# Kernel optimization log

Measured on AMD Instinct MI355X. Metric: run time of the kernel, lower is better.

The kernel has to match this reference:

```python
import jax, jax.numpy as jnp
import numpy as np

G = 32          # num graphs
NPG = 512       # nodes per graph
EPG = 4096      # edges per graph
DN = 128        # node/edge feat dim
DP = 64         # node identifier dim d_p
DE_ID = 64      # type identifier dim d_e
H = 768         # hidden_dim
IN_DIM = DN + 2 * DP + DE_ID  # 320


def setup_inputs() -> dict:
    key = jax.random.key(0)
    ks = jax.random.split(key, 9)
    N = G * NPG
    E = G * EPG
    x = jax.random.normal(ks[0], (N, DN), jnp.float32)
    edge_attr = jax.random.normal(ks[1], (E, DN), jnp.float32)
    P = jax.random.normal(ks[2], (N, DP), jnp.float32)  # ORF node identifiers
    E_V = jax.random.normal(ks[3], (1, DE_ID), jnp.float32) * 0.1
    E_E = jax.random.normal(ks[4], (1, DE_ID), jnp.float32) * 0.1
    W = jax.random.normal(ks[5], (H, IN_DIM), jnp.float32) / np.sqrt(IN_DIM)
    b = jnp.zeros((H,), jnp.float32)
    graph_token = jax.random.normal(ks[6], (1, H), jnp.float32) * 0.1
    # edges stay within their graph and are sorted by graph id
    base = jnp.repeat(jnp.arange(G, dtype=jnp.int32) * NPG, EPG)  # [E]
    src = base + jax.random.randint(ks[7], (E,), 0, NPG, jnp.int32)
    dst = base + jax.random.randint(ks[8], (E,), 0, NPG, jnp.int32)
    edge_index = jnp.stack([src, dst], axis=0)  # [2, E]
    batch = jnp.repeat(jnp.arange(G, dtype=jnp.int32), NPG)  # [N]
    return {
        "x": x, "edge_attr": edge_attr, "P": P,
        "E_V": E_V, "E_E": E_E, "W": W, "b": b, "graph_token": graph_token,
        "edge_index": edge_index, "batch": batch,
        "num_graphs": G, "max_node_num": NPG, "max_edge_num": EPG,
    }


def reference(x, edge_attr, P, E_V, E_E, W, b, graph_token,
              edge_index, batch, num_graphs, max_node_num, max_edge_num):
    N = x.shape[0]
    E = edge_index.shape[1]
    Hd = W.shape[0]
    d_e = E_V.shape[1]

    # node tokens: [x | P | P | E_V] @ W^T + b
    X_v = jnp.concatenate([x, P, P, jnp.broadcast_to(E_V, (N, d_e))], axis=1)
    X_v_proj = X_v @ W.T + b  # [N, H]

    # edge tokens: [edge_attr | P_u | P_v | E_E] @ W^T + b
    P_u = P[edge_index[0]]
    P_v = P[edge_index[1]]
    X_e = jnp.concatenate([edge_attr, P_u, P_v, jnp.broadcast_to(E_E, (E, d_e))], axis=1)
    X_e_proj = X_e @ W.T + b  # [E, H]

    # ragged -> padded packing (replaces per-graph python loop)
    ones_n = jnp.ones((N,), jnp.int32)
    node_num = jax.ops.segment_sum(ones_n, batch, num_segments=num_graphs)  # [G]
    node_ptr = jnp.cumsum(node_num) - node_num  # exclusive prefix sum
    node_pos = jnp.arange(N, dtype=jnp.int32) - node_ptr[batch]  # position within graph

    edge_batch = batch[edge_index[0]]  # [E]
    ones_e = jnp.ones((E,), jnp.int32)
    edge_num = jax.ops.segment_sum(ones_e, edge_batch, num_segments=num_graphs)
    edge_ptr = jnp.cumsum(edge_num) - edge_num
    edge_pos = jnp.arange(E, dtype=jnp.int32) - edge_ptr[edge_batch]

    seq_len = 1 + max_node_num + max_edge_num  # +1 for [graph] token
    tokens = jnp.zeros((num_graphs, seq_len, Hd), X_v_proj.dtype)
    tokens = tokens.at[:, 0, :].set(graph_token[0])
    tokens = tokens.at[batch, 1 + node_pos].set(X_v_proj)
    tokens = tokens.at[edge_batch, 1 + max_node_num + edge_pos].set(X_e_proj)

    attention_masks = jnp.zeros((num_graphs, seq_len), bool)
    attention_masks = attention_masks.at[:, 0].set(True)
    attention_masks = attention_masks.at[batch, 1 + node_pos].set(True)
    attention_masks = attention_masks.at[edge_batch, 1 + max_node_num + edge_pos].set(True)

    return tokens, attention_masks
```

## Files before the change

kernel.cpp:

```cpp
#include <hip/hip_runtime.h>
#include <stdint.h>

#define NG   32
#define NPG  512
#define EPG  4096
#define DN   128
#define DP   64
#define NN   (NG*NPG)
#define NE   (NG*EPG)
#define KD   320
#define HD   768
#define SEQ  (1+NPG+EPG)
#define TOK_ELEMS ((size_t)NG*SEQ*HD)
#define MASK_ELEMS ((size_t)NG*SEQ)

typedef unsigned short u16;
typedef __attribute__((ext_vector_type(8))) __bf16 bf16x8;
typedef __attribute__((ext_vector_type(8))) short  s16x8;
typedef __attribute__((ext_vector_type(4))) float  f32x4;

__device__ __forceinline__ u16 f2bf(float f) {
    uint32_t u = __builtin_bit_cast(uint32_t, f);
    u += 0x7fffu + ((u >> 16) & 1u);
    return (u16)(u >> 16);
}

__device__ __forceinline__ int b_off(int row, int kb) {
    return ((row >> 1) << 7) + ((row & 1) << 6) + (kb ^ (((row >> 1) & 3) << 4));
}

__global__ void ptr_k(const int* __restrict__ batch, const int* __restrict__ eidx,
                      int* __restrict__ nptr, int* __restrict__ eptr) {
    int t = threadIdx.x;
    if (t < NG) {
        int g = t, lo = 0, hi = NN;
        while (lo < hi) { int mid = (lo + hi) >> 1; if (batch[mid] < g) lo = mid + 1; else hi = mid; }
        nptr[g] = lo;
    } else if (t < 2 * NG) {
        int g = t - NG, lo = 0, hi = NE;
        while (lo < hi) { int mid = (lo + hi) >> 1; if (batch[eidx[mid]] < g) lo = mid + 1; else hi = mid; }
        eptr[g] = lo;
    }
}

__global__ void wconv_k(const float* __restrict__ W, u16* __restrict__ Wb) {
    int i = blockIdx.x * 256 + threadIdx.x;
    if (i < KD * HD) Wb[i] = f2bf(W[i]);
}

__global__ void aux_k(const float* __restrict__ gt, float* __restrict__ out) {
    size_t i = (size_t)blockIdx.x * 256 + threadIdx.x;
    if (i < (size_t)NG * HD) {
        int g = (int)(i / HD), c = (int)(i % HD);
        out[(size_t)g * SEQ * HD + c] = gt[c];
    } else {
        size_t m = i - (size_t)NG * HD;
        if (m < MASK_ELEMS) out[TOK_ELEMS + m] = 1.0f;
    }
}

__global__ __launch_bounds__(256, 2)
void gemm_scatter(const float* __restrict__ x,  const float* __restrict__ ea,
                  const float* __restrict__ P,  const float* __restrict__ EV,
                  const float* __restrict__ EEv,const float* __restrict__ bias,
                  const int* __restrict__ eidx, const int* __restrict__ batch,
                  const u16* __restrict__ Wb,   const int* __restrict__ nptr,
                  const int* __restrict__ eptr, float* __restrict__ out)
{
    __shared__ __align__(16) char b_lds[2][16384];
    __shared__ int info_src[128], info_pu[128], info_pv[128], info_orow[128];

    const int tid  = threadIdx.x;
    const int lane = tid & 63;
    const int wid  = tid >> 6;
    const int lrow = lane & 15;
    const int lq   = lane >> 4;

    uint32_t g_off[4], l_off[4];
    #pragma unroll
    for (int i = 0; i < 4; ++i) {
        uint32_t u = (uint32_t)(i * 256 + tid);
        g_off[i] = (u >> 3) * (KD * 2) + (u & 7) * 16;
        l_off[i] = (((u >> 2) & 1) * 8192u) + (uint32_t)b_off(u >> 3, (u & 3) * 16);
    }
    const char* WbB = (const char*)Wb;

    const int r0  = blockIdx.x * 128;
    const bool isNode = (r0 < NN);
    const float* feat = isNode ? x  : ea;
    const float* idv  = isNode ? EV : EEv;

    if (tid < 128) {
        int r = r0 + tid;
        if (isNode) {
            int g = batch[r];
            info_src[tid] = r; info_pu[tid] = r; info_pv[tid] = r;
            info_orow[tid] = g * SEQ + 1 + (r - nptr[g]);
        } else {
            int e = r - NN;
            int s = eidx[e], d = eidx[NE + e];
            int g = batch[s];
            info_src[tid] = e; info_pu[tid] = s; info_pv[tid] = d;
            info_orow[tid] = g * SEQ + 1 + NPG + (e - eptr[g]);
        }
    }
    __syncthreads();

    bf16x8 afr[2][10];
    int obase[2][4];
    #pragma unroll
    for (int rb = 0; rb < 2; ++rb) {
        const int arow = wid * 32 + rb * 16 + lrow;
        const int fsrc = info_src[arow];
        const int pu   = info_pu[arow];
        const int pv   = info_pv[arow];
        #pragma unroll
        for (int s = 0; s < 10; ++s) {
            const int kg = s * 32 + lq * 8;
            const float* sp;
            if      (s < 4) sp = feat + (size_t)fsrc * DN + kg;
            else if (s < 6) sp = P + (size_t)pu * DP + (kg - DN);
            else if (s < 8) sp = P + (size_t)pv * DP + (kg - DN - DP);
            else            sp = idv + (kg - DN - 2 * DP);
            f32x4 f0 = *reinterpret_cast<const f32x4*>(sp);
            f32x4 f1 = *reinterpret_cast<const f32x4*>(sp + 4);
            s16x8 v;
            v[0]=(short)f2bf(f0[0]); v[1]=(short)f2bf(f0[1]);
            v[2]=(short)f2bf(f0[2]); v[3]=(short)f2bf(f0[3]);
            v[4]=(short)f2bf(f1[0]); v[5]=(short)f2bf(f1[1]);
            v[6]=(short)f2bf(f1[2]); v[7]=(short)f2bf(f1[3]);
            afr[rb][s] = __builtin_bit_cast(bf16x8, v);
        }
        #pragma unroll
        for (int j = 0; j < 4; ++j)
            obase[rb][j] = info_orow[wid * 32 + rb * 16 + lq * 4 + j] * HD;
    }

    const int roff = b_off(lrow, lq * 16);

    s16x8 pre[4];
    #pragma unroll
    for (int i = 0; i < 4; ++i)
        pre[i] = *reinterpret_cast<const s16x8*>(WbB + g_off[i]);

    int cur = 0;
    int nxt = 1;
    for (int nt = 0; nt < 6; ++nt) {
        const int n0 = nt * 128;
        f32x4 acc[2][8];
        #pragma unroll
        for (int rb = 0; rb < 2; ++rb)
            #pragma unroll
            for (int i = 0; i < 8; ++i) acc[rb][i] = (f32x4)0.f;

        #pragma unroll
        for (int kp = 0; kp < 5; ++kp) {
            cur ^= 1;
            char* bb = &b_lds[0][0] + cur * 16384;
            #pragma unroll
            for (int i = 0; i < 4; ++i)
                *reinterpret_cast<s16x8*>(bb + l_off[i]) = pre[i];
            {
                int tn  = (nxt < 30) ? nxt : 29; ++nxt;
                int ntn = tn / 5, kpn = tn - ntn * 5;
                const char* gb = WbB + (size_t)ntn * (128 * KD * 2) + kpn * 128;
                #pragma unroll
                for (int i = 0; i < 4; ++i)
                    pre[i] = *reinterpret_cast<const s16x8*>(gb + g_off[i]);
            }
            asm volatile("s_waitcnt lgkmcnt(0)" ::: "memory");
            __builtin_amdgcn_sched_barrier(0);
            __builtin_amdgcn_s_barrier();
            #pragma unroll
            for (int kk = 0; kk < 2; ++kk) {
                const int kt = kp * 2 + kk;
                const char* bs = bb + kk * 8192;
                #pragma unroll
                for (int ni = 0; ni < 8; ++ni) {
                    bf16x8 bf = *reinterpret_cast<const bf16x8*>(bs + ni * 1024 + roff);
                    acc[0][ni] = __builtin_amdgcn_mfma_f32_16x16x32_bf16(afr[0][kt], bf, acc[0][ni], 0, 0, 0);
                    acc[1][ni] = __builtin_amdgcn_mfma_f32_16x16x32_bf16(afr[1][kt], bf, acc[1][ni], 0, 0, 0);
                }
            }
        }

        #pragma unroll
        for (int ni = 0; ni < 8; ++ni) {
            float bv = bias[n0 + ni * 16 + lrow];
            #pragma unroll
            for (int rb = 0; rb < 2; ++rb)
                #pragma unroll
                for (int j = 0; j < 4; ++j)
                    out[obase[rb][j] + n0 + ni * 16 + lrow] = acc[rb][ni][j] + bv;
        }
    }
}

extern "C" void kernel_launch(void* const* d_in, const int* in_sizes, int n_in,
                              void* d_out, int out_size, void* d_ws, size_t ws_size,
                              hipStream_t stream) {
    const float* x    = (const float*)d_in[0];
    const float* ea   = (const float*)d_in[1];
    const float* P    = (const float*)d_in[2];
    const float* EV   = (const float*)d_in[3];
    const float* EEv  = (const float*)d_in[4];
    const float* W    = (const float*)d_in[5];
    const float* bias = (const float*)d_in[6];
    const float* gt   = (const float*)d_in[7];
    const int* eidx   = (const int*)d_in[8];
    const int* batch  = (const int*)d_in[9];

    float* out = (float*)d_out;
    u16* Wb  = (u16*)d_ws;
    int* ints = (int*)((char*)d_ws + (size_t)KD * HD * 2);
    int *nptr = ints, *eptr = ints + 32;

    ptr_k<<<1, 64, 0, stream>>>(batch, eidx, nptr, eptr);
    wconv_k<<<(KD * HD + 255) / 256, 256, 0, stream>>>(W, Wb);
    aux_k<<<(int)(((size_t)NG * HD + MASK_ELEMS + 255) / 256), 256, 0, stream>>>(gt, out);
    gemm_scatter<<<dim3((NN + NE) / 128), 256, 0, stream>>>(
        x, ea, P, EV, EEv, bias, eidx, batch, Wb, nptr, eptr, out);
}
```

Baseline: 169.3 us.

## Halve N-tile to 64 and interleave previous tile's stores with next tile's MFMAs

The GEMM N-tile shrinks from 128 to 64 columns, so the LDS B buffer is halved and the prefetch schedule now walks 60 stages instead of 30. Two accumulator sets ping-pong, and the epilogue stores of the previous 64-column tile are spread across the five k-steps of the current tile, so global writes overlap MFMA work instead of forming a separate store burst. This is meant to hide the large output-write cost, at the price of more barriers per block and less B reuse per LDS load.

After: 169.0 us. Within noise of the previous version (-0.2%).

```diff
diff --git a/kernel.cpp b/kernel.cpp
--- a/kernel.cpp
+++ b/kernel.cpp
@@ -67,7 +67,7 @@
                   const u16* __restrict__ Wb,   const int* __restrict__ nptr,
                   const int* __restrict__ eptr, float* __restrict__ out)
 {
-    __shared__ __align__(16) char b_lds[2][16384];
+    __shared__ __align__(16) char b_lds[2][8192];
     __shared__ int info_src[128], info_pu[128], info_pv[128], info_orow[128];
 
     const int tid  = threadIdx.x;
@@ -76,12 +76,13 @@
     const int lrow = lane & 15;
     const int lq   = lane >> 4;
 
-    uint32_t g_off[4], l_off[4];
-    #pragma unroll
-    for (int i = 0; i < 4; ++i) {
+    uint32_t g_off[2], l_off[2];
+    #pragma unroll
+    for (int i = 0; i < 2; ++i) {
         uint32_t u = (uint32_t)(i * 256 + tid);
-        g_off[i] = (u >> 3) * (KD * 2) + (u & 7) * 16;
-        l_off[i] = (((u >> 2) & 1) * 8192u) + (uint32_t)b_off(u >> 3, (u & 3) * 16);
+        uint32_t row = u >> 3, c = u & 7;
+        g_off[i] = row * (KD * 2) + c * 16;
+        l_off[i] = ((c >> 2) * 4096u) + (uint32_t)b_off((int)row, (int)((c & 3) * 16));
     }
     const char* WbB = (const char*)Wb;
 
@@ -138,34 +139,41 @@
 
     const int roff = b_off(lrow, lq * 16);
 
-    s16x8 pre[4];
-    #pragma unroll
-    for (int i = 0; i < 4; ++i)
+    s16x8 pre[2];
+    #pragma unroll
+    for (int i = 0; i < 2; ++i)
         pre[i] = *reinterpret_cast<const s16x8*>(WbB + g_off[i]);
 
     int cur = 0;
     int nxt = 1;
-    for (int nt = 0; nt < 6; ++nt) {
-        const int n0 = nt * 128;
-        f32x4 acc[2][8];
+
+    constexpr int S0[5] = {0, 7, 14, 20, 26};
+    constexpr int S1[5] = {7, 14, 20, 26, 32};
+
+    auto do_nt = [&](f32x4 (&acc)[2][4], float (&bv)[4],
+                     f32x4 (&accP)[2][4], float (&bvP)[4],
+                     int n0, int pn0) {
         #pragma unroll
         for (int rb = 0; rb < 2; ++rb)
             #pragma unroll
-            for (int i = 0; i < 8; ++i) acc[rb][i] = (f32x4)0.f;
+            for (int i = 0; i < 4; ++i) acc[rb][i] = (f32x4)0.f;
+        #pragma unroll
+        for (int ni = 0; ni < 4; ++ni)
+            bv[ni] = bias[n0 + ni * 16 + lrow];
 
         #pragma unroll
         for (int kp = 0; kp < 5; ++kp) {
             cur ^= 1;
-            char* bb = &b_lds[0][0] + cur * 16384;
+            char* bb = &b_lds[0][0] + cur * 8192;
             #pragma unroll
-            for (int i = 0; i < 4; ++i)
+            for (int i = 0; i < 2; ++i)
                 *reinterpret_cast<s16x8*>(bb + l_off[i]) = pre[i];
             {
-                int tn  = (nxt < 30) ? nxt : 29; ++nxt;
+                int tn  = (nxt < 60) ? nxt : 59; ++nxt;
                 int ntn = tn / 5, kpn = tn - ntn * 5;
-                const char* gb = WbB + (size_t)ntn * (128 * KD * 2) + kpn * 128;
+                const char* gb = WbB + (size_t)ntn * (64 * KD * 2) + kpn * 128;
                 #pragma unroll
-                for (int i = 0; i < 4; ++i)
+                for (int i = 0; i < 2; ++i)
                     pre[i] = *reinterpret_cast<const s16x8*>(gb + g_off[i]);
             }
             asm volatile("s_waitcnt lgkmcnt(0)" ::: "memory");
@@ -174,25 +182,40 @@
             #pragma unroll
             for (int kk = 0; kk < 2; ++kk) {
                 const int kt = kp * 2 + kk;
-                const char* bs = bb + kk * 8192;
+                const char* bs = bb + kk * 4096;
                 #pragma unroll
-                for (int ni = 0; ni < 8; ++ni) {
+                for (int ni = 0; ni < 4; ++ni) {
                     bf16x8 bf = *reinterpret_cast<const bf16x8*>(bs + ni * 1024 + roff);
                     acc[0][ni] = __builtin_amdgcn_mfma_f32_16x16x32_bf16(afr[0][kt], bf, acc[0][ni], 0, 0, 0);
                     acc[1][ni] = __builtin_amdgcn_mfma_f32_16x16x32_bf16(afr[1][kt], bf, acc[1][ni], 0, 0, 0);
                 }
             }
+            if (pn0 >= 0) {
+                #pragma unroll
+                for (int si = S0[kp]; si < S1[kp]; ++si) {
+                    const int j  = si & 3;
+                    const int rb = (si >> 2) & 1;
+                    const int ni = si >> 3;
+                    out[(size_t)(obase[rb][j] + pn0 + ni * 16 + lrow)] =
+                        accP[rb][ni][j] + bvP[ni];
+                }
+            }
         }
-
-        #pragma unroll
-        for (int ni = 0; ni < 8; ++ni) {
-            float bv = bias[n0 + ni * 16 + lrow];
-            #pragma unroll
-            for (int rb = 0; rb < 2; ++rb)
-                #pragma unroll
-                for (int j = 0; j < 4; ++j)
-                    out[obase[rb][j] + n0 + ni * 16 + lrow] = acc[rb][ni][j] + bv;
-        }
+    };
+
+    f32x4 accA[2][4], accB[2][4];
+    float bvA[4], bvB[4];
+    #pragma unroll
+    for (int p = 0; p < 6; ++p) {
+        do_nt(accA, bvA, accB, bvB, (2 * p) * 64,     2 * p * 64 - 64);
+        do_nt(accB, bvB, accA, bvA, (2 * p + 1) * 64, (2 * p + 1) * 64 - 64);
+    }
+    #pragma unroll
+    for (int si = 0; si < 32; ++si) {
+        const int j  = si & 3;
+        const int rb = (si >> 2) & 1;
+        const int ni = si >> 3;
+        out[(size_t)(obase[rb][j] + 704 + ni * 16 + lrow)] = accB[rb][ni][j] + bvB[ni];
     }
 }
 
```
